# Kernel tuning notes

Hardware: AMD Instinct MI355X
Metric: run time of the kernel (lower is better)

## Reference

```python
import jax, jax.numpy as jnp
import numpy as np

B, N, T, DIN = 64, 512, 8, 2
H, L, E, M, P = 256, 3, 8192, 128, 12
EPS = 1e-5


def setup_inputs() -> dict:
    key = jax.random.key(0)
    ks = jax.random.split(key, 10)
    obs_traj = jax.random.normal(ks[0], (B, N, T, DIN), dtype=jnp.float32)
    nodes = jax.random.randint(ks[1], (B, 1, E), 0, N)
    edges = jax.random.randint(ks[2], (B, 1, E), 0, M)
    hyperedge_indices = jnp.concatenate([nodes, edges], axis=1)  # [B,2,E]
    s = 0.05
    return {
        "obs_traj": obs_traj,
        "hyperedge_indices": hyperedge_indices,
        "W_enc": jax.random.normal(ks[3], (DIN, H), dtype=jnp.float32) * s,
        "b_enc": jnp.zeros((H,), dtype=jnp.float32),
        "thetas": jax.random.normal(ks[4], (L, H, H), dtype=jnp.float32) * s,
        "conv_biases": jnp.zeros((L, H), dtype=jnp.float32),
        "gammas": jnp.ones((L, H), dtype=jnp.float32),
        "betas": jnp.zeros((L, H), dtype=jnp.float32),
        "W_dec": jax.random.normal(ks[5], (H, P * 2), dtype=jnp.float32) * s,
        "b_dec": jnp.zeros((P * 2,), dtype=jnp.float32),
    }


def _hconv(x, idx, theta, bias):
    # PyG HypergraphConv: out = D^{-1} H B^{-1} H^T (X Theta) + bias
    # x: [N,H], idx: [2,E] (row0 node ids, row1 hyperedge ids)
    nodes, edges = idx[0], idx[1]
    xt = x @ theta  # [N,H]
    ones = jnp.ones((idx.shape[1],), dtype=x.dtype)
    b_deg = jax.ops.segment_sum(ones, edges, num_segments=M)  # hyperedge degree [M]
    d_deg = jax.ops.segment_sum(ones, nodes, num_segments=N)  # node degree [N]
    msg = jax.ops.segment_sum(xt[nodes], edges, num_segments=M)  # [M,H]
    msg = msg / jnp.maximum(b_deg, 1.0)[:, None]
    out = jax.ops.segment_sum(msg[edges], nodes, num_segments=N)  # [N,H]
    out = out / jnp.maximum(d_deg, 1.0)[:, None]
    return out + bias


def reference(obs_traj, hyperedge_indices, W_enc, b_enc, thetas, conv_biases,
              gammas, betas, W_dec, b_dec):
    # TemporalEncoder: per-step linear + ReLU, mean over time -> [B,N,H]
    h = jnp.mean(jax.nn.relu(obs_traj @ W_enc + b_enc), axis=2)
    h_social = h
    for l in range(L):
        conv = jax.vmap(lambda x, idx: _hconv(x, idx, thetas[l], conv_biases[l]))
        hc = conv(h_social, hyperedge_indices)  # [B,N,H]
        # BatchNorm1d applied per sample (training-mode stats over node dim)
        mu = jnp.mean(hc, axis=1, keepdims=True)
        var = jnp.var(hc, axis=1, keepdims=True)
        hn = (hc - mu) * jax.lax.rsqrt(var + EPS) * gammas[l] + betas[l]
        h_social = jax.nn.relu(hn)  # dropout = identity (eval)
    h_combined = h + h_social
    out = h_combined @ W_dec + b_dec  # [B,N,P*2]
    return out.reshape(B, N, P, 2)
```

## Files before the change

### kernel.cpp

```cpp
#include <hip/hip_runtime.h>
#include <hip/hip_bf16.h>

#define B_   64
#define N_   512
#define T_   8
#define DIN_ 2
#define H_   256
#define L_   3
#define E_   8192
#define M_   128
#define P2_  24
#define EPS_ 1e-5f

#define TILE 64
#define KC   16
#define WTPAD 136

typedef __attribute__((ext_vector_type(8))) short short8;
typedef __attribute__((ext_vector_type(4))) float floatx4;

__device__ __forceinline__ unsigned short f2bf(float f) {
    union { float f; unsigned u; } v; v.f = f;
    unsigned r = v.u + 0x7FFF + ((v.u >> 16) & 1);
    return (unsigned short)(r >> 16);
}
__device__ __forceinline__ float bf2f(unsigned short h) {
    union { unsigned u; float f; } v; v.u = (unsigned)h << 16; return v.f;
}

__global__ __launch_bounds__(512, 2) void prep_kernel(
    const float* __restrict__ obs, const float* __restrict__ Wenc,
    const float* __restrict__ benc, float* __restrict__ hT,
    unsigned short* __restrict__ actT, long actLo,
    const int* __restrict__ idx, unsigned short* __restrict__ Hmat,
    unsigned short* __restrict__ HmatT, float* __restrict__ DinvN,
    float* __restrict__ degM,
    const float* __restrict__ thetas, unsigned short* __restrict__ thT, long thLo)
{
    __shared__ __align__(16) char u[33024];
    int bid = blockIdx.x, tid = threadIdx.x;
    if (bid < 256) {
        float* ot = (float*)u;
        int b = bid >> 2, h0 = (bid & 3) * 64;
        const float4* src = (const float4*)(obs + (long)b * N_ * 16);
        for (int i = tid; i < 2048; i += 512) {
            float4 v = src[i];
            int n = i >> 2, k4 = (i & 3) << 2;
            ot[(k4 + 0) * 513 + n] = v.x;
            ot[(k4 + 1) * 513 + n] = v.y;
            ot[(k4 + 2) * 513 + n] = v.z;
            ot[(k4 + 3) * 513 + n] = v.w;
        }
        __syncthreads();
        int wave = tid >> 6, lane = tid & 63;
        int cbase = h0 + wave * 8;
        float w0[8], w1[8], bb[8];
#pragma unroll
        for (int i = 0; i < 8; ++i) {
            w0[i] = Wenc[cbase + i];
            w1[i] = Wenc[H_ + cbase + i];
            bb[i] = benc[cbase + i];
        }
        for (int j = 0; j < 8; ++j) {
            int n = j * 64 + lane;
            float x0[8], x1[8];
#pragma unroll
            for (int t = 0; t < 8; ++t) {
                x0[t] = ot[(2 * t) * 513 + n];
                x1[t] = ot[(2 * t + 1) * 513 + n];
            }
#pragma unroll
            for (int i = 0; i < 8; ++i) {
                float acc = 0.f;
#pragma unroll
                for (int t = 0; t < 8; ++t)
                    acc += fmaxf(x0[t] * w0[i] + x1[t] * w1[i] + bb[i], 0.f);
                acc *= 0.125f;
                long o = ((long)b * H_ + cbase + i) * N_ + n;
                hT[o] = acc;
                unsigned short hv = f2bf(acc);
                actT[o] = hv;
                actT[actLo + o] = f2bf(acc - bf2f(hv));
            }
        }
    } else if (bid < 768) {
        unsigned* cnt = (unsigned*)u;
        int id2 = bid - 256;
        int b = id2 >> 3, chunk = id2 & 7;
        int c0 = chunk * 64;
        for (int i = tid; i < 64 * 129; i += 512) cnt[i] = 0;
        __syncthreads();
        const int* nodes = idx + (long)b * 2 * E_;
        const int* edges = nodes + E_;
        for (int e = tid; e < E_; e += 512) {
            int n = nodes[e];
            if ((n >> 6) == chunk) atomicAdd(&cnt[(n & 63) * 129 + edges[e]], 1u);
        }
        __syncthreads();
        for (int i = tid; i < 64 * 128; i += 512) {
            int r = i >> 7, m = i & 127;
            Hmat[((long)(b * N_ + c0 + r)) * M_ + m] = f2bf((float)cnt[r * 129 + m]);
        }
        for (int i = tid; i < 64 * 128; i += 512) {
            int m = i >> 6, r = i & 63;
            HmatT[((long)(b * M_ + m)) * N_ + c0 + r] = f2bf((float)cnt[r * 129 + m]);
        }
        if (tid < 64) {
            unsigned s = 0;
#pragma unroll 8
            for (int m = 0; m < 128; ++m) s += cnt[tid * 129 + m];
            DinvN[b * N_ + c0 + tid] = 1.0f / fmaxf((float)s, 1.0f);
        } else if (tid < 192) {
            int m = tid - 64;
            unsigned s = 0;
#pragma unroll 8
            for (int r = 0; r < 64; ++r) s += cnt[r * 129 + m];
            atomicAdd(&degM[b * M_ + m], (float)s);
        }
    } else {
        float (*tile)[65] = (float(*)[65])u;
        int sub = bid - 768;
        int cx = sub & 3, ry = (sub >> 2) & 3, l = sub >> 4;
        int r0 = ry * 64, c0 = cx * 64;
        const float* ib = thetas + (long)l * H_ * H_;
        unsigned short* ob = thT + (long)l * H_ * H_;
        int x = tid & 63, y0 = tid >> 6;
#pragma unroll
        for (int i = 0; i < 8; ++i) {
            int y = y0 * 8 + i;
            tile[y][x] = ib[(long)(r0 + y) * H_ + c0 + x];
        }
        __syncthreads();
#pragma unroll
        for (int i = 0; i < 8; ++i) {
            int y = y0 * 8 + i;
            float v = tile[x][y];
            unsigned short hv = f2bf(v);
            long o = (long)(c0 + y) * H_ + r0 + x;
            ob[o] = hv;
            ob[thLo + o] = f2bf(v - bf2f(hv));
        }
    }
}

__global__ __launch_bounds__(256, 2) void z_kernel(
    const unsigned short* __restrict__ HmatT,
    const unsigned short* __restrict__ actIn, long actLo,
    const float* __restrict__ degM,
    unsigned short* __restrict__ Zg, long zLo)
{
    __shared__ __align__(16) unsigned short As1[128 * 40];
    __shared__ __align__(16) unsigned short Bh[128 * 40];
    __shared__ __align__(16) unsigned short Bl[128 * 40];
    int b = blockIdx.x, hs = blockIdx.y * 128;
    int tid = threadIdx.x, wave = tid >> 6, lane = tid & 63;
    int lr = lane & 15, lq = lane >> 4;
    int wm = (wave & 1) * 64, wn = (wave >> 1) * 64;
    const unsigned short* HT   = HmatT + (long)b * M_ * N_;
    const unsigned short* aInH = actIn + (long)b * H_ * N_ + (long)hs * N_;
    const unsigned short* aInL = actIn + actLo + (long)b * H_ * N_ + (long)hs * N_;

    floatx4 acc[4][4] = {};
    int r0 = tid >> 2, ck = (tid & 3) << 3;
    int r1 = (tid + 256) >> 2;
    uint4 pA0  = *(const uint4*)&HT[(long)r0 * N_ + ck];
    uint4 pA1  = *(const uint4*)&HT[(long)r1 * N_ + ck];
    uint4 pBh0 = *(const uint4*)&aInH[(long)r0 * N_ + ck];
    uint4 pBh1 = *(const uint4*)&aInH[(long)r1 * N_ + ck];
    uint4 pBl0 = *(const uint4*)&aInL[(long)r0 * N_ + ck];
    uint4 pBl1 = *(const uint4*)&aInL[(long)r1 * N_ + ck];
    for (int k0 = 0; k0 < N_; k0 += 32) {
        __syncthreads();
        *(uint4*)&As1[r0 * 40 + ck] = pA0;
        *(uint4*)&As1[r1 * 40 + ck] = pA1;
        *(uint4*)&Bh[r0 * 40 + ck]  = pBh0;
        *(uint4*)&Bh[r1 * 40 + ck]  = pBh1;
        *(uint4*)&Bl[r0 * 40 + ck]  = pBl0;
        *(uint4*)&Bl[r1 * 40 + ck]  = pBl1;
        __syncthreads();
        int kn = k0 + 32;
        if (kn < N_) {
            pA0  = *(const uint4*)&HT[(long)r0 * N_ + kn + ck];
            pA1  = *(const uint4*)&HT[(long)r1 * N_ + kn + ck];
            pBh0 = *(const uint4*)&aInH[(long)r0 * N_ + kn + ck];
            pBh1 = *(const uint4*)&aInH[(long)r1 * N_ + kn + ck];
            pBl0 = *(const uint4*)&aInL[(long)r0 * N_ + kn + ck];
            pBl1 = *(const uint4*)&aInL[(long)r1 * N_ + kn + ck];
        }
        short8 af[4], bh[4], bl[4];
#pragma unroll
        for (int mt = 0; mt < 4; ++mt)
            af[mt] = *(const short8*)&As1[(wm + mt * 16 + lr) * 40 + lq * 8];
#pragma unroll
        for (int nt = 0; nt < 4; ++nt) {
            bh[nt] = *(const short8*)&Bh[(wn + nt * 16 + lr) * 40 + lq * 8];
            bl[nt] = *(const short8*)&Bl[(wn + nt * 16 + lr) * 40 + lq * 8];
        }
#pragma unroll
        for (int mt = 0; mt < 4; ++mt)
#pragma unroll
            for (int nt = 0; nt < 4; ++nt) {
                acc[mt][nt] = __builtin_amdgcn_mfma_f32_16x16x32_bf16(
                    af[mt], bh[nt], acc[mt][nt], 0, 0, 0);
                acc[mt][nt] = __builtin_amdgcn_mfma_f32_16x16x32_bf16(
                    af[mt], bl[nt], acc[mt][nt], 0, 0, 0);
            }
    }
#pragma unroll
    for (int mt = 0; mt < 4; ++mt)
#pragma unroll
        for (int r4 = 0; r4 < 4; ++r4) {
            int m = wm + mt * 16 + lq * 4 + r4;
            float rsB = 1.0f / fmaxf(degM[b * M_ + m], 1.0f);
#pragma unroll
            for (int nt = 0; nt < 4; ++nt) {
                float v = acc[mt][nt][r4] * rsB;
                unsigned short hv = f2bf(v);
                long o = ((long)b * M_ + m) * H_ + hs + wn + nt * 16 + lr;
                Zg[o] = hv;
                Zg[zLo + o] = f2bf(v - bf2f(hv));
            }
        }
}

__global__ __launch_bounds__(512, 2) void wh_kernel(
    const unsigned short* __restrict__ Zg, long zLo,
    const unsigned short* __restrict__ Hmat,
    const unsigned short* __restrict__ thT, long thLo,
    const float* __restrict__ DinvN, const float* __restrict__ convb,
    const float* __restrict__ gamma, const float* __restrict__ beta,
    unsigned short* __restrict__ actOut, long actLo)
{
    __shared__ __align__(16) char lds[39424];
    unsigned short* Zch  = (unsigned short*)lds;
    unsigned short* Zcl  = Zch + 128 * 40;
    unsigned short* As2h = Zcl + 128 * 40;
    unsigned short* As2l = As2h + 64 * 40;
    unsigned short* Wh   = (unsigned short*)lds;
    unsigned short* Wl   = Wh + 64 * WTPAD;
    float* rsum = (float*)(lds + 64 * WTPAD * 2 * 2);
    float* rsq  = rsum + 512;
    float2* prm = (float2*)(rsq + 512);

    int id = blockIdx.x + (blockIdx.y << 2);
    int xcd = id & 7, slot = id >> 3;
    int b  = ((slot >> 2) << 3) + xcd;
    int h0 = (slot & 3) * 64;

    int tid = threadIdx.x, wave = tid >> 6, lane = tid & 63;
    int lr = lane & 15, lq = lane >> 4;
    const unsigned short* Zb = Zg + (long)b * M_ * H_;
    const unsigned short* Hm = Hmat + (long)b * N_ * M_;

    int wm2 = (wave >> 2) * 32, wn2 = (wave & 3) * 32;
    int i2 = tid & 255, pl2 = tid >> 8;
    int r2 = i2 >> 2, ck2 = (i2 & 3) << 3;
    const unsigned short* thBase = thT + (pl2 ? thLo : 0) + (long)(h0 + r2) * H_ + ck2;
    unsigned short* As2dst = (pl2 ? As2l : As2h) + r2 * 40 + ck2;
    int rz = tid >> 2, ckz = (tid & 3) << 3;
    uint4 pTh = *(const uint4*)thBase;
    uint4 pZh = *(const uint4*)&Zb[(long)rz * H_ + ckz];
    uint4 pZl = *(const uint4*)&Zb[zLo + (long)rz * H_ + ckz];
    floatx4 acc2[2][2] = {};
    for (int k0 = 0; k0 < H_; k0 += 32) {
        __syncthreads();
        *(uint4*)As2dst = pTh;
        *(uint4*)&Zch[rz * 40 + ckz] = pZh;
        *(uint4*)&Zcl[rz * 40 + ckz] = pZl;
        __syncthreads();
        int kn = k0 + 32;
        if (kn < H_) {
            pTh = *(const uint4*)(thBase + kn);
            pZh = *(const uint4*)&Zb[(long)rz * H_ + kn + ckz];
            pZl = *(const uint4*)&Zb[zLo + (long)rz * H_ + kn + ckz];
        }
        short8 ah[2], al[2], zb[2], zl[2];
#pragma unroll
        for (int mt = 0; mt < 2; ++mt) {
            ah[mt] = *(const short8*)&As2h[(wm2 + mt * 16 + lr) * 40 + lq * 8];
            al[mt] = *(const short8*)&As2l[(wm2 + mt * 16 + lr) * 40 + lq * 8];
        }
#pragma unroll
        for (int nt = 0; nt < 2; ++nt) {
            zb[nt] = *(const short8*)&Zch[(wn2 + nt * 16 + lr) * 40 + lq * 8];
            zl[nt] = *(const short8*)&Zcl[(wn2 + nt * 16 + lr) * 40 + lq * 8];
        }
#pragma unroll
        for (int mt = 0; mt < 2; ++mt)
#pragma unroll
            for (int nt = 0; nt < 2; ++nt) {
                acc2[mt][nt] = __builtin_amdgcn_mfma_f32_16x16x32_bf16(
                    ah[mt], zb[nt], acc2[mt][nt], 0, 0, 0);
                acc2[mt][nt] = __builtin_amdgcn_mfma_f32_16x16x32_bf16(
                    ah[mt], zl[nt], acc2[mt][nt], 0, 0, 0);
                acc2[mt][nt] = __builtin_amdgcn_mfma_f32_16x16x32_bf16(
                    al[mt], zb[nt], acc2[mt][nt], 0, 0, 0);
            }
    }
    __syncthreads();
#pragma unroll
    for (int mt = 0; mt < 2; ++mt)
#pragma unroll
        for (int r4 = 0; r4 < 4; ++r4) {
            int row = wm2 + mt * 16 + lq * 4 + r4;
#pragma unroll
            for (int nt = 0; nt < 2; ++nt) {
                int col = wn2 + nt * 16 + lr;
                float v = acc2[mt][nt][r4];
                unsigned short hv = f2bf(v);
                Wh[row * WTPAD + col] = hv;
                Wl[row * WTPAD + col] = f2bf(v - bf2f(hv));
            }
        }
    __syncthreads();

    int wn3 = wave * 64;
    floatx4 acc3[4][4] = {};
    for (int k0 = 0; k0 < M_; k0 += 32) {
        short8 ah[4], al[4], bh3[4];
#pragma unroll
        for (int nt = 0; nt < 4; ++nt)
            bh3[nt] = *(const short8*)&Hm[(long)(wn3 + nt * 16 + lr) * M_ + k0 + lq * 8];
#pragma unroll
        for (int mt = 0; mt < 4; ++mt) {
            ah[mt] = *(const short8*)&Wh[(mt * 16 + lr) * WTPAD + k0 + lq * 8];
            al[mt] = *(const short8*)&Wl[(mt * 16 + lr) * WTPAD + k0 + lq * 8];
        }
#pragma unroll
        for (int mt = 0; mt < 4; ++mt)
#pragma unroll
            for (int nt = 0; nt < 4; ++nt) {
                acc3[mt][nt] = __builtin_amdgcn_mfma_f32_16x16x32_bf16(
                    ah[mt], bh3[nt], acc3[mt][nt], 0, 0, 0);
                acc3[mt][nt] = __builtin_amdgcn_mfma_f32_16x16x32_bf16(
                    al[mt], bh3[nt], acc3[mt][nt], 0, 0, 0);
            }
    }

    float dv[4];
#pragma unroll
    for (int nt = 0; nt < 4; ++nt)
        dv[nt] = DinvN[b * N_ + wn3 + nt * 16 + lr];
    float cb[4][4];
#pragma unroll
    for (int mt = 0; mt < 4; ++mt)
#pragma unroll
        for (int r4 = 0; r4 < 4; ++r4)
            cb[mt][r4] = convb[h0 + mt * 16 + lq * 4 + r4];
#pragma unroll
    for (int mt = 0; mt < 4; ++mt)
#pragma unroll
        for (int nt = 0; nt < 4; ++nt)
#pragma unroll
            for (int r4 = 0; r4 < 4; ++r4)
                acc3[mt][nt][r4] = acc3[mt][nt][r4] * dv[nt] + cb[mt][r4];

    float ps[4][4], pq[4][4];
#pragma unroll
    for (int mt = 0; mt < 4; ++mt)
#pragma unroll
        for (int r4 = 0; r4 < 4; ++r4) {
            float s = 0.f, q = 0.f;
#pragma unroll
            for (int nt = 0; nt < 4; ++nt) {
                float v = acc3[mt][nt][r4];
                s += v; q += v * v;
            }
            ps[mt][r4] = s; pq[mt][r4] = q;
        }
#pragma unroll
    for (int mask = 1; mask <= 8; mask <<= 1) {
#pragma unroll
        for (int mt = 0; mt < 4; ++mt)
#pragma unroll
            for (int r4 = 0; r4 < 4; ++r4) {
                ps[mt][r4] += __shfl_xor(ps[mt][r4], mask);
                pq[mt][r4] += __shfl_xor(pq[mt][r4], mask);
            }
    }
    if (lr == 0) {
#pragma unroll
        for (int mt = 0; mt < 4; ++mt)
#pragma unroll
            for (int r4 = 0; r4 < 4; ++r4) {
                int row = mt * 16 + lq * 4 + r4;
                rsum[row * 8 + wave] = ps[mt][r4];
                rsq[row * 8 + wave]  = pq[mt][r4];
            }
    }
    __syncthreads();
    if (tid < 64) {
        float s = 0.f, s2 = 0.f;
#pragma unroll
        for (int w = 0; w < 8; ++w) { s += rsum[tid * 8 + w]; s2 += rsq[tid * 8 + w]; }
        float mu  = s * (1.0f / N_);
        float var = fmaxf(s2 * (1.0f / N_) - mu * mu, 0.f);
        float sc  = gamma[h0 + tid] * rsqrtf(var + EPS_);
        prm[tid] = make_float2(sc, beta[h0 + tid] - mu * sc);
    }
    __syncthreads();

    unsigned short* ab = actOut + (long)b * H_ * N_;
#pragma unroll
    for (int mt = 0; mt < 4; ++mt)
#pragma unroll
        for (int r4 = 0; r4 < 4; ++r4) {
            int row = mt * 16 + lq * 4 + r4;
            float2 p = prm[row];
#pragma unroll
            for (int nt = 0; nt < 4; ++nt) {
                float y = fmaxf(acc3[mt][nt][r4] * p.x + p.y, 0.f);
                unsigned short hv = f2bf(y);
                long o = (long)(h0 + row) * N_ + wn3 + nt * 16 + lr;
                ab[o] = hv;
                ab[actLo + o] = f2bf(y - bf2f(hv));
            }
        }
}

__global__ __launch_bounds__(256) void comb_transpose_kernel(
    const unsigned short* __restrict__ actT, long actLo,
    const float* __restrict__ hT, float* __restrict__ comb)
{
    int b  = blockIdx.z;
    int n0 = blockIdx.x * 64, h0 = blockIdx.y * 64;
    __shared__ float tile[64][65];
    const unsigned short* ab = actT + (long)b * H_ * N_;
    const float* hb = hT + (long)b * H_ * N_;
    int x = threadIdx.x & 63, y0 = threadIdx.x >> 6;
#pragma unroll
    for (int i = 0; i < 16; ++i) {
        int y = y0 * 16 + i;
        long o = (long)(h0 + y) * N_ + n0 + x;
        tile[y][x] = bf2f(ab[o]) + bf2f(ab[actLo + o]) + hb[o];
    }
    __syncthreads();
#pragma unroll
    for (int i = 0; i < 16; ++i) {
        int y = y0 * 16 + i;
        comb[((long)b * N_ + n0 + y) * H_ + h0 + x] = tile[x][y];
    }
}

__global__ __launch_bounds__(256) void gemm_kernel(
    const float* __restrict__ A, long aStride,
    const float* __restrict__ Bm, long bStride,
    float* __restrict__ C, long cStride,
    int M, int Nn, int K,
    const float* __restrict__ bias)
{
    int b  = blockIdx.z;
    int m0 = blockIdx.y * TILE;
    int n0 = blockIdx.x * TILE;
    const float* Ab = A + (long)b * aStride;
    const float* Bb = Bm + (long)b * bStride;
    float*       Cb = C + (long)b * cStride;

    __shared__ float As[KC][TILE];
    __shared__ float Bs[KC][TILE];

    int tid = threadIdx.x;
    int tx4 = (tid & 15) << 2;
    int ty4 = (tid >> 4) << 2;
    int lr  = tid >> 2;
    int lc4 = (tid & 3) << 2;
    int br  = tid >> 4;
    int bc4 = (tid & 15) << 2;

    float acc[4][4] = {};

    for (int k0 = 0; k0 < K; k0 += KC) {
        float4 av = *(const float4*)(Ab + (long)(m0 + lr) * K + k0 + lc4);
        As[lc4 + 0][lr] = av.x;
        As[lc4 + 1][lr] = av.y;
        As[lc4 + 2][lr] = av.z;
        As[lc4 + 3][lr] = av.w;
        int cc = n0 + bc4;
        float4 bv = make_float4(0.f, 0.f, 0.f, 0.f);
        const float* bp = Bb + (long)(k0 + br) * Nn + cc;
        if (cc + 3 < Nn) {
            bv = *(const float4*)bp;
        } else {
            if (cc + 0 < Nn) bv.x = bp[0];
            if (cc + 1 < Nn) bv.y = bp[1];
            if (cc + 2 < Nn) bv.z = bp[2];
            if (cc + 3 < Nn) bv.w = bp[3];
        }
        *(float4*)&Bs[br][bc4] = bv;
        __syncthreads();
#pragma unroll
        for (int kk = 0; kk < KC; ++kk) {
            float4 a  = *(const float4*)&As[kk][ty4];
            float4 bq = *(const float4*)&Bs[kk][tx4];
            acc[0][0] += a.x * bq.x; acc[0][1] += a.x * bq.y;
            acc[0][2] += a.x * bq.z; acc[0][3] += a.x * bq.w;
            acc[1][0] += a.y * bq.x; acc[1][1] += a.y * bq.y;
            acc[1][2] += a.y * bq.z; acc[1][3] += a.y * bq.w;
            acc[2][0] += a.z * bq.x; acc[2][1] += a.z * bq.y;
            acc[2][2] += a.z * bq.z; acc[2][3] += a.z * bq.w;
            acc[3][0] += a.w * bq.x; acc[3][1] += a.w * bq.y;
            acc[3][2] += a.w * bq.z; acc[3][3] += a.w * bq.w;
        }
        __syncthreads();
    }

#pragma unroll
    for (int i = 0; i < 4; ++i) {
        int r = m0 + ty4 + i;
#pragma unroll
        for (int j = 0; j < 4; ++j) {
            int c = n0 + tx4 + j;
            if (c < Nn)
                Cb[(long)r * Nn + c] = acc[i][j] + (bias ? bias[c] : 0.f);
        }
    }
}

extern "C" void kernel_launch(void* const* d_in, const int* in_sizes, int n_in,
                              void* d_out, int out_size, void* d_ws, size_t ws_size,
                              hipStream_t stream) {
    const float* obs    = (const float*)d_in[0];
    const int*   hyper  = (const int*)d_in[1];
    const float* Wenc   = (const float*)d_in[2];
    const float* benc   = (const float*)d_in[3];
    const float* thetas = (const float*)d_in[4];
    const float* convb  = (const float*)d_in[5];
    const float* gammas = (const float*)d_in[6];
    const float* betas  = (const float*)d_in[7];
    const float* Wdec   = (const float*)d_in[8];
    const float* bdec   = (const float*)d_in[9];
    float* out = (float*)d_out;

    char* w = (char*)d_ws;
    auto alloc = [&](size_t bytes) { char* p = w; w += (bytes + 255) & ~255ULL; return p; };
    float* hT    = (float*)alloc((size_t)B_ * H_ * N_ * 4);
    float* comb  = (float*)alloc((size_t)B_ * N_ * H_ * 4);
    float* DinvN = (float*)alloc((size_t)B_ * N_ * 4);
    float* degM  = (float*)alloc((size_t)B_ * M_ * 4);
    unsigned short* Hmat  = (unsigned short*)alloc((size_t)B_ * N_ * M_ * 2);
    unsigned short* HmatT = (unsigned short*)alloc((size_t)B_ * M_ * N_ * 2);
    unsigned short* actA  = (unsigned short*)alloc((size_t)B_ * H_ * N_ * 2 * 2);
    unsigned short* actB  = (unsigned short*)alloc((size_t)B_ * H_ * N_ * 2 * 2);
    unsigned short* thT   = (unsigned short*)alloc((size_t)L_ * H_ * H_ * 2 * 2);
    unsigned short* Zg    = (unsigned short*)alloc((size_t)B_ * M_ * H_ * 2 * 2);

    const long actLo = (long)B_ * H_ * N_;
    const long thLo  = (long)L_ * H_ * H_;
    const long zLo   = (long)B_ * M_ * H_;

    hipMemsetAsync(degM, 0, (size_t)B_ * M_ * 4, stream);
    prep_kernel<<<816, 512, 0, stream>>>(
        obs, Wenc, benc, hT, actA, actLo,
        hyper, Hmat, HmatT, DinvN, degM,
        thetas, thT, thLo);

    const unsigned short* cur = actA;
    unsigned short* nxt = actB;
    for (int l = 0; l < L_; ++l) {
        z_kernel<<<dim3(B_, 2), 256, 0, stream>>>(
            HmatT, cur, actLo, degM, Zg, zLo);
        wh_kernel<<<dim3(4, B_), 512, 0, stream>>>(
            Zg, zLo, Hmat, thT + (size_t)l * H_ * H_, thLo,
            DinvN, convb + (size_t)l * H_,
            gammas + (size_t)l * H_, betas + (size_t)l * H_, nxt, actLo);
        const unsigned short* t = cur; cur = nxt; nxt = (unsigned short*)t;
    }
    comb_transpose_kernel<<<dim3(8, 4, B_), 256, 0, stream>>>(cur, actLo, hT, comb);
    gemm_kernel<<<dim3(1, N_ / TILE, B_), 256, 0, stream>>>(
        comb, (long)N_ * H_, Wdec, 0,
        out, (long)N_ * P2_, N_, P2_, H_, bdec);
}
```

Measured before the change: 269.4 us.

## Halve z/wh tile widths for more blocks and fuse decoder with combine-transpose

Result: faster. 229.0 us (-15.0%).

```diff
diff --git a/kernel.cpp b/kernel.cpp
--- a/kernel.cpp
+++ b/kernel.cpp
@@ -12,8 +12,6 @@
 #define P2_  24
 #define EPS_ 1e-5f
 
-#define TILE 64
-#define KC   16
 #define WTPAD 136
 
 typedef __attribute__((ext_vector_type(8))) short short8;
@@ -143,63 +141,57 @@
     }
 }
 
-__global__ __launch_bounds__(256, 2) void z_kernel(
+__global__ __launch_bounds__(256, 4) void z_kernel(
     const unsigned short* __restrict__ HmatT,
     const unsigned short* __restrict__ actIn, long actLo,
     const float* __restrict__ degM,
     unsigned short* __restrict__ Zg, long zLo)
 {
     __shared__ __align__(16) unsigned short As1[128 * 40];
-    __shared__ __align__(16) unsigned short Bh[128 * 40];
-    __shared__ __align__(16) unsigned short Bl[128 * 40];
-    int b = blockIdx.x, hs = blockIdx.y * 128;
+    __shared__ __align__(16) unsigned short Bh[64 * 40];
+    __shared__ __align__(16) unsigned short Bl[64 * 40];
+    int b = blockIdx.x, hs = blockIdx.y * 64;
     int tid = threadIdx.x, wave = tid >> 6, lane = tid & 63;
     int lr = lane & 15, lq = lane >> 4;
-    int wm = (wave & 1) * 64, wn = (wave >> 1) * 64;
+    int wm = (wave & 1) * 64, wn = (wave >> 1) * 32;
     const unsigned short* HT   = HmatT + (long)b * M_ * N_;
     const unsigned short* aInH = actIn + (long)b * H_ * N_ + (long)hs * N_;
     const unsigned short* aInL = actIn + actLo + (long)b * H_ * N_ + (long)hs * N_;
 
-    floatx4 acc[4][4] = {};
+    floatx4 acc[4][2] = {};
     int r0 = tid >> 2, ck = (tid & 3) << 3;
-    int r1 = (tid + 256) >> 2;
-    uint4 pA0  = *(const uint4*)&HT[(long)r0 * N_ + ck];
-    uint4 pA1  = *(const uint4*)&HT[(long)r1 * N_ + ck];
-    uint4 pBh0 = *(const uint4*)&aInH[(long)r0 * N_ + ck];
-    uint4 pBh1 = *(const uint4*)&aInH[(long)r1 * N_ + ck];
-    uint4 pBl0 = *(const uint4*)&aInL[(long)r0 * N_ + ck];
-    uint4 pBl1 = *(const uint4*)&aInL[(long)r1 * N_ + ck];
+    int r1 = r0 + 64;
+    uint4 pA0 = *(const uint4*)&HT[(long)r0 * N_ + ck];
+    uint4 pA1 = *(const uint4*)&HT[(long)r1 * N_ + ck];
+    uint4 pBh = *(const uint4*)&aInH[(long)r0 * N_ + ck];
+    uint4 pBl = *(const uint4*)&aInL[(long)r0 * N_ + ck];
     for (int k0 = 0; k0 < N_; k0 += 32) {
         __syncthreads();
         *(uint4*)&As1[r0 * 40 + ck] = pA0;
         *(uint4*)&As1[r1 * 40 + ck] = pA1;
-        *(uint4*)&Bh[r0 * 40 + ck]  = pBh0;
-        *(uint4*)&Bh[r1 * 40 + ck]  = pBh1;
-        *(uint4*)&Bl[r0 * 40 + ck]  = pBl0;
-        *(uint4*)&Bl[r1 * 40 + ck]  = pBl1;
+        *(uint4*)&Bh[r0 * 40 + ck]  = pBh;
+        *(uint4*)&Bl[r0 * 40 + ck]  = pBl;
         __syncthreads();
         int kn = k0 + 32;
         if (kn < N_) {
-            pA0  = *(const uint4*)&HT[(long)r0 * N_ + kn + ck];
-            pA1  = *(const uint4*)&HT[(long)r1 * N_ + kn + ck];
-            pBh0 = *(const uint4*)&aInH[(long)r0 * N_ + kn + ck];
-            pBh1 = *(const uint4*)&aInH[(long)r1 * N_ + kn + ck];
-            pBl0 = *(const uint4*)&aInL[(long)r0 * N_ + kn + ck];
-            pBl1 = *(const uint4*)&aInL[(long)r1 * N_ + kn + ck];
-        }
-        short8 af[4], bh[4], bl[4];
+            pA0 = *(const uint4*)&HT[(long)r0 * N_ + kn + ck];
+            pA1 = *(const uint4*)&HT[(long)r1 * N_ + kn + ck];
+            pBh = *(const uint4*)&aInH[(long)r0 * N_ + kn + ck];
+            pBl = *(const uint4*)&aInL[(long)r0 * N_ + kn + ck];
+        }
+        short8 af[4], bh[2], bl[2];
 #pragma unroll
         for (int mt = 0; mt < 4; ++mt)
             af[mt] = *(const short8*)&As1[(wm + mt * 16 + lr) * 40 + lq * 8];
 #pragma unroll
-        for (int nt = 0; nt < 4; ++nt) {
+        for (int nt = 0; nt < 2; ++nt) {
             bh[nt] = *(const short8*)&Bh[(wn + nt * 16 + lr) * 40 + lq * 8];
             bl[nt] = *(const short8*)&Bl[(wn + nt * 16 + lr) * 40 + lq * 8];
         }
 #pragma unroll
         for (int mt = 0; mt < 4; ++mt)
 #pragma unroll
-            for (int nt = 0; nt < 4; ++nt) {
+            for (int nt = 0; nt < 2; ++nt) {
                 acc[mt][nt] = __builtin_amdgcn_mfma_f32_16x16x32_bf16(
                     af[mt], bh[nt], acc[mt][nt], 0, 0, 0);
                 acc[mt][nt] = __builtin_amdgcn_mfma_f32_16x16x32_bf16(
@@ -213,7 +205,7 @@
             int m = wm + mt * 16 + lq * 4 + r4;
             float rsB = 1.0f / fmaxf(degM[b * M_ + m], 1.0f);
 #pragma unroll
-            for (int nt = 0; nt < 4; ++nt) {
+            for (int nt = 0; nt < 2; ++nt) {
                 float v = acc[mt][nt][r4] * rsB;
                 unsigned short hv = f2bf(v);
                 long o = ((long)b * M_ + m) * H_ + hs + wn + nt * 16 + lr;
@@ -223,7 +215,7 @@
         }
 }
 
-__global__ __launch_bounds__(512, 2) void wh_kernel(
+__global__ __launch_bounds__(512, 4) void wh_kernel(
     const unsigned short* __restrict__ Zg, long zLo,
     const unsigned short* __restrict__ Hmat,
     const unsigned short* __restrict__ thT, long thLo,
@@ -231,103 +223,96 @@
     const float* __restrict__ gamma, const float* __restrict__ beta,
     unsigned short* __restrict__ actOut, long actLo)
 {
-    __shared__ __align__(16) char lds[39424];
+    __shared__ __align__(16) char lds[28160];
     unsigned short* Zch  = (unsigned short*)lds;
     unsigned short* Zcl  = Zch + 128 * 40;
     unsigned short* As2h = Zcl + 128 * 40;
-    unsigned short* As2l = As2h + 64 * 40;
+    unsigned short* As2l = As2h + 32 * 40;
     unsigned short* Wh   = (unsigned short*)lds;
-    unsigned short* Wl   = Wh + 64 * WTPAD;
-    float* rsum = (float*)(lds + 64 * WTPAD * 2 * 2);
-    float* rsq  = rsum + 512;
-    float2* prm = (float2*)(rsq + 512);
-
-    int id = blockIdx.x + (blockIdx.y << 2);
+    unsigned short* Wl   = Wh + 32 * WTPAD;
+    float* rsum = (float*)(lds + 25600);
+    float* rsq  = rsum + 256;
+    float2* prm = (float2*)(rsq + 256);
+
+    int id = blockIdx.x;
     int xcd = id & 7, slot = id >> 3;
-    int b  = ((slot >> 2) << 3) + xcd;
-    int h0 = (slot & 3) * 64;
+    int chunk = slot & 7;
+    int b  = ((slot >> 3) << 3) | xcd;
+    int h0 = chunk * 32;
 
     int tid = threadIdx.x, wave = tid >> 6, lane = tid & 63;
     int lr = lane & 15, lq = lane >> 4;
     const unsigned short* Zb = Zg + (long)b * M_ * H_;
     const unsigned short* Hm = Hmat + (long)b * N_ * M_;
 
-    int wm2 = (wave >> 2) * 32, wn2 = (wave & 3) * 32;
+    int wm2 = (wave >> 2) * 16, wn2 = (wave & 3) * 32;
     int i2 = tid & 255, pl2 = tid >> 8;
     int r2 = i2 >> 2, ck2 = (i2 & 3) << 3;
+    bool thAct = (i2 < 128);
     const unsigned short* thBase = thT + (pl2 ? thLo : 0) + (long)(h0 + r2) * H_ + ck2;
     unsigned short* As2dst = (pl2 ? As2l : As2h) + r2 * 40 + ck2;
     int rz = tid >> 2, ckz = (tid & 3) << 3;
-    uint4 pTh = *(const uint4*)thBase;
+    uint4 pTh = {};
+    if (thAct) pTh = *(const uint4*)thBase;
     uint4 pZh = *(const uint4*)&Zb[(long)rz * H_ + ckz];
     uint4 pZl = *(const uint4*)&Zb[zLo + (long)rz * H_ + ckz];
-    floatx4 acc2[2][2] = {};
+    floatx4 acc2[2] = {};
     for (int k0 = 0; k0 < H_; k0 += 32) {
         __syncthreads();
-        *(uint4*)As2dst = pTh;
+        if (thAct) *(uint4*)As2dst = pTh;
         *(uint4*)&Zch[rz * 40 + ckz] = pZh;
         *(uint4*)&Zcl[rz * 40 + ckz] = pZl;
         __syncthreads();
         int kn = k0 + 32;
         if (kn < H_) {
-            pTh = *(const uint4*)(thBase + kn);
+            if (thAct) pTh = *(const uint4*)(thBase + kn);
             pZh = *(const uint4*)&Zb[(long)rz * H_ + kn + ckz];
             pZl = *(const uint4*)&Zb[zLo + (long)rz * H_ + kn + ckz];
         }
-        short8 ah[2], al[2], zb[2], zl[2];
-#pragma unroll
-        for (int mt = 0; mt < 2; ++mt) {
-            ah[mt] = *(const short8*)&As2h[(wm2 + mt * 16 + lr) * 40 + lq * 8];
-            al[mt] = *(const short8*)&As2l[(wm2 + mt * 16 + lr) * 40 + lq * 8];
-        }
+        short8 ah, al, zb[2], zl[2];
+        ah = *(const short8*)&As2h[(wm2 + lr) * 40 + lq * 8];
+        al = *(const short8*)&As2l[(wm2 + lr) * 40 + lq * 8];
 #pragma unroll
         for (int nt = 0; nt < 2; ++nt) {
             zb[nt] = *(const short8*)&Zch[(wn2 + nt * 16 + lr) * 40 + lq * 8];
             zl[nt] = *(const short8*)&Zcl[(wn2 + nt * 16 + lr) * 40 + lq * 8];
         }
 #pragma unroll
-        for (int mt = 0; mt < 2; ++mt)
-#pragma unroll
-            for (int nt = 0; nt < 2; ++nt) {
-                acc2[mt][nt] = __builtin_amdgcn_mfma_f32_16x16x32_bf16(
-                    ah[mt], zb[nt], acc2[mt][nt], 0, 0, 0);
-                acc2[mt][nt] = __builtin_amdgcn_mfma_f32_16x16x32_bf16(
-                    ah[mt], zl[nt], acc2[mt][nt], 0, 0, 0);
-                acc2[mt][nt] = __builtin_amdgcn_mfma_f32_16x16x32_bf16(
-                    al[mt], zb[nt], acc2[mt][nt], 0, 0, 0);
-            }
+        for (int nt = 0; nt < 2; ++nt) {
+            acc2[nt] = __builtin_amdgcn_mfma_f32_16x16x32_bf16(ah, zb[nt], acc2[nt], 0, 0, 0);
+            acc2[nt] = __builtin_amdgcn_mfma_f32_16x16x32_bf16(ah, zl[nt], acc2[nt], 0, 0, 0);
+            acc2[nt] = __builtin_amdgcn_mfma_f32_16x16x32_bf16(al, zb[nt], acc2[nt], 0, 0, 0);
+        }
     }
     __syncthreads();
 #pragma unroll
-    for (int mt = 0; mt < 2; ++mt)
-#pragma unroll
-        for (int r4 = 0; r4 < 4; ++r4) {
-            int row = wm2 + mt * 16 + lq * 4 + r4;
-#pragma unroll
-            for (int nt = 0; nt < 2; ++nt) {
-                int col = wn2 + nt * 16 + lr;
-                float v = acc2[mt][nt][r4];
-                unsigned short hv = f2bf(v);
-                Wh[row * WTPAD + col] = hv;
-                Wl[row * WTPAD + col] = f2bf(v - bf2f(hv));
-            }
-        }
+    for (int r4 = 0; r4 < 4; ++r4) {
+        int row = wm2 + lq * 4 + r4;
+#pragma unroll
+        for (int nt = 0; nt < 2; ++nt) {
+            int col = wn2 + nt * 16 + lr;
+            float v = acc2[nt][r4];
+            unsigned short hv = f2bf(v);
+            Wh[row * WTPAD + col] = hv;
+            Wl[row * WTPAD + col] = f2bf(v - bf2f(hv));
+        }
+    }
     __syncthreads();
 
     int wn3 = wave * 64;
-    floatx4 acc3[4][4] = {};
+    floatx4 acc3[2][4] = {};
     for (int k0 = 0; k0 < M_; k0 += 32) {
-        short8 ah[4], al[4], bh3[4];
+        short8 ah[2], al[2], bh3[4];
 #pragma unroll
         for (int nt = 0; nt < 4; ++nt)
             bh3[nt] = *(const short8*)&Hm[(long)(wn3 + nt * 16 + lr) * M_ + k0 + lq * 8];
 #pragma unroll
-        for (int mt = 0; mt < 4; ++mt) {
+        for (int mt = 0; mt < 2; ++mt) {
             ah[mt] = *(const short8*)&Wh[(mt * 16 + lr) * WTPAD + k0 + lq * 8];
             al[mt] = *(const short8*)&Wl[(mt * 16 + lr) * WTPAD + k0 + lq * 8];
         }
 #pragma unroll
-        for (int mt = 0; mt < 4; ++mt)
+        for (int mt = 0; mt < 2; ++mt)
 #pragma unroll
             for (int nt = 0; nt < 4; ++nt) {
                 acc3[mt][nt] = __builtin_amdgcn_mfma_f32_16x16x32_bf16(
@@ -341,23 +326,23 @@
 #pragma unroll
     for (int nt = 0; nt < 4; ++nt)
         dv[nt] = DinvN[b * N_ + wn3 + nt * 16 + lr];
-    float cb[4][4];
-#pragma unroll
-    for (int mt = 0; mt < 4; ++mt)
+    float cb[2][4];
+#pragma unroll
+    for (int mt = 0; mt < 2; ++mt)
 #pragma unroll
         for (int r4 = 0; r4 < 4; ++r4)
             cb[mt][r4] = convb[h0 + mt * 16 + lq * 4 + r4];
 #pragma unroll
-    for (int mt = 0; mt < 4; ++mt)
+    for (int mt = 0; mt < 2; ++mt)
 #pragma unroll
         for (int nt = 0; nt < 4; ++nt)
 #pragma unroll
             for (int r4 = 0; r4 < 4; ++r4)
                 acc3[mt][nt][r4] = acc3[mt][nt][r4] * dv[nt] + cb[mt][r4];
 
-    float ps[4][4], pq[4][4];
-#pragma unroll
-    for (int mt = 0; mt < 4; ++mt)
+    float ps[2][4], pq[2][4];
+#pragma unroll
+    for (int mt = 0; mt < 2; ++mt)
 #pragma unroll
         for (int r4 = 0; r4 < 4; ++r4) {
             float s = 0.f, q = 0.f;
@@ -371,7 +356,7 @@
 #pragma unroll
     for (int mask = 1; mask <= 8; mask <<= 1) {
 #pragma unroll
-        for (int mt = 0; mt < 4; ++mt)
+        for (int mt = 0; mt < 2; ++mt)
 #pragma unroll
             for (int r4 = 0; r4 < 4; ++r4) {
                 ps[mt][r4] += __shfl_xor(ps[mt][r4], mask);
@@ -380,7 +365,7 @@
     }
     if (lr == 0) {
 #pragma unroll
-        for (int mt = 0; mt < 4; ++mt)
+        for (int mt = 0; mt < 2; ++mt)
 #pragma unroll
             for (int r4 = 0; r4 < 4; ++r4) {
                 int row = mt * 16 + lq * 4 + r4;
@@ -389,7 +374,7 @@
             }
     }
     __syncthreads();
-    if (tid < 64) {
+    if (tid < 32) {
         float s = 0.f, s2 = 0.f;
 #pragma unroll
         for (int w = 0; w < 8; ++w) { s += rsum[tid * 8 + w]; s2 += rsq[tid * 8 + w]; }
@@ -402,7 +387,7 @@
 
     unsigned short* ab = actOut + (long)b * H_ * N_;
 #pragma unroll
-    for (int mt = 0; mt < 4; ++mt)
+    for (int mt = 0; mt < 2; ++mt)
 #pragma unroll
         for (int r4 = 0; r4 < 4; ++r4) {
             int row = mt * 16 + lq * 4 + r4;
@@ -418,102 +403,50 @@
         }
 }
 
-__global__ __launch_bounds__(256) void comb_transpose_kernel(
+__global__ __launch_bounds__(256, 2) void decoder_kernel(
     const unsigned short* __restrict__ actT, long actLo,
-    const float* __restrict__ hT, float* __restrict__ comb)
+    const float* __restrict__ hT,
+    const float* __restrict__ Wdec, const float* __restrict__ bdec,
+    float* __restrict__ out)
 {
-    int b  = blockIdx.z;
-    int n0 = blockIdx.x * 64, h0 = blockIdx.y * 64;
-    __shared__ float tile[64][65];
+    __shared__ float ct[64 * 65];
+    __shared__ float wd[256 * 25];
+    int n0 = blockIdx.x * 64, b = blockIdx.y;
+    int tid = threadIdx.x;
+    for (int i = tid; i < 256 * 24; i += 256)
+        wd[(i / 24) * 25 + (i % 24)] = Wdec[i];
+
     const unsigned short* ab = actT + (long)b * H_ * N_;
     const float* hb = hT + (long)b * H_ * N_;
-    int x = threadIdx.x & 63, y0 = threadIdx.x >> 6;
-#pragma unroll
-    for (int i = 0; i < 16; ++i) {
-        int y = y0 * 16 + i;
-        long o = (long)(h0 + y) * N_ + n0 + x;
-        tile[y][x] = bf2f(ab[o]) + bf2f(ab[actLo + o]) + hb[o];
-    }
-    __syncthreads();
-#pragma unroll
-    for (int i = 0; i < 16; ++i) {
-        int y = y0 * 16 + i;
-        comb[((long)b * N_ + n0 + y) * H_ + h0 + x] = tile[x][y];
-    }
-}
-
-__global__ __launch_bounds__(256) void gemm_kernel(
-    const float* __restrict__ A, long aStride,
-    const float* __restrict__ Bm, long bStride,
-    float* __restrict__ C, long cStride,
-    int M, int Nn, int K,
-    const float* __restrict__ bias)
-{
-    int b  = blockIdx.z;
-    int m0 = blockIdx.y * TILE;
-    int n0 = blockIdx.x * TILE;
-    const float* Ab = A + (long)b * aStride;
-    const float* Bb = Bm + (long)b * bStride;
-    float*       Cb = C + (long)b * cStride;
-
-    __shared__ float As[KC][TILE];
-    __shared__ float Bs[KC][TILE];
-
-    int tid = threadIdx.x;
-    int tx4 = (tid & 15) << 2;
-    int ty4 = (tid >> 4) << 2;
-    int lr  = tid >> 2;
-    int lc4 = (tid & 3) << 2;
-    int br  = tid >> 4;
-    int bc4 = (tid & 15) << 2;
-
-    float acc[4][4] = {};
-
-    for (int k0 = 0; k0 < K; k0 += KC) {
-        float4 av = *(const float4*)(Ab + (long)(m0 + lr) * K + k0 + lc4);
-        As[lc4 + 0][lr] = av.x;
-        As[lc4 + 1][lr] = av.y;
-        As[lc4 + 2][lr] = av.z;
-        As[lc4 + 3][lr] = av.w;
-        int cc = n0 + bc4;
-        float4 bv = make_float4(0.f, 0.f, 0.f, 0.f);
-        const float* bp = Bb + (long)(k0 + br) * Nn + cc;
-        if (cc + 3 < Nn) {
-            bv = *(const float4*)bp;
-        } else {
-            if (cc + 0 < Nn) bv.x = bp[0];
-            if (cc + 1 < Nn) bv.y = bp[1];
-            if (cc + 2 < Nn) bv.z = bp[2];
-            if (cc + 3 < Nn) bv.w = bp[3];
-        }
-        *(float4*)&Bs[br][bc4] = bv;
-        __syncthreads();
-#pragma unroll
-        for (int kk = 0; kk < KC; ++kk) {
-            float4 a  = *(const float4*)&As[kk][ty4];
-            float4 bq = *(const float4*)&Bs[kk][tx4];
-            acc[0][0] += a.x * bq.x; acc[0][1] += a.x * bq.y;
-            acc[0][2] += a.x * bq.z; acc[0][3] += a.x * bq.w;
-            acc[1][0] += a.y * bq.x; acc[1][1] += a.y * bq.y;
-            acc[1][2] += a.y * bq.z; acc[1][3] += a.y * bq.w;
-            acc[2][0] += a.z * bq.x; acc[2][1] += a.z * bq.y;
-            acc[2][2] += a.z * bq.z; acc[2][3] += a.z * bq.w;
-            acc[3][0] += a.w * bq.x; acc[3][1] += a.w * bq.y;
-            acc[3][2] += a.w * bq.z; acc[3][3] += a.w * bq.w;
-        }
-        __syncthreads();
-    }
-
-#pragma unroll
-    for (int i = 0; i < 4; ++i) {
-        int r = m0 + ty4 + i;
-#pragma unroll
-        for (int j = 0; j < 4; ++j) {
-            int c = n0 + tx4 + j;
-            if (c < Nn)
-                Cb[(long)r * Nn + c] = acc[i][j] + (bias ? bias[c] : 0.f);
-        }
-    }
+    int x = tid & 63, y0 = tid >> 6;
+
+    int n = tid >> 2;
+    int p0 = (tid & 3) * 6;
+    float acc[6] = {};
+
+    for (int k0 = 0; k0 < H_; k0 += 64) {
+        __syncthreads();
+#pragma unroll
+        for (int i = 0; i < 16; ++i) {
+            int y = y0 * 16 + i;
+            long o = (long)(k0 + y) * N_ + n0 + x;
+            ct[x * 65 + y] = hb[o] + bf2f(ab[o]) + bf2f(ab[actLo + o]);
+        }
+        __syncthreads();
+        const float* crow = &ct[n * 65];
+#pragma unroll 8
+        for (int kk = 0; kk < 64; ++kk) {
+            float a = crow[kk];
+            const float* wrow = &wd[(k0 + kk) * 25 + p0];
+#pragma unroll
+            for (int j = 0; j < 6; ++j)
+                acc[j] += a * wrow[j];
+        }
+    }
+    long ob = ((long)b * N_ + n0 + n) * P2_ + p0;
+#pragma unroll
+    for (int j = 0; j < 6; ++j)
+        out[ob + j] = acc[j] + bdec[p0 + j];
 }
 
 extern "C" void kernel_launch(void* const* d_in, const int* in_sizes, int n_in,
@@ -534,7 +467,6 @@
     char* w = (char*)d_ws;
     auto alloc = [&](size_t bytes) { char* p = w; w += (bytes + 255) & ~255ULL; return p; };
     float* hT    = (float*)alloc((size_t)B_ * H_ * N_ * 4);
-    float* comb  = (float*)alloc((size_t)B_ * N_ * H_ * 4);
     float* DinvN = (float*)alloc((size_t)B_ * N_ * 4);
     float* degM  = (float*)alloc((size_t)B_ * M_ * 4);
     unsigned short* Hmat  = (unsigned short*)alloc((size_t)B_ * N_ * M_ * 2);
@@ -557,16 +489,14 @@
     const unsigned short* cur = actA;
     unsigned short* nxt = actB;
     for (int l = 0; l < L_; ++l) {
-        z_kernel<<<dim3(B_, 2), 256, 0, stream>>>(
+        z_kernel<<<dim3(B_, 4), 256, 0, stream>>>(
             HmatT, cur, actLo, degM, Zg, zLo);
-        wh_kernel<<<dim3(4, B_), 512, 0, stream>>>(
+        wh_kernel<<<512, 512, 0, stream>>>(
             Zg, zLo, Hmat, thT + (size_t)l * H_ * H_, thLo,
             DinvN, convb + (size_t)l * H_,
             gammas + (size_t)l * H_, betas + (size_t)l * H_, nxt, actLo);
         const unsigned short* t = cur; cur = nxt; nxt = (unsigned short*)t;
     }
-    comb_transpose_kernel<<<dim3(8, 4, B_), 256, 0, stream>>>(cur, actLo, hT, comb);
-    gemm_kernel<<<dim3(1, N_ / TILE, B_), 256, 0, stream>>>(
-        comb, (long)N_ * H_, Wdec, 0,
-        out, (long)N_ * P2_, N_, P2_, H_, bdec);
-}
+    decoder_kernel<<<dim3(8, B_), 256, 0, stream>>>(
+        cur, actLo, hT, Wdec, bdec, out);
+}
```
